# Optimization experiments

Measured on AMD Instinct MI355X. Metric: run time of the kernel, lower is better.

Reference implementation:

```python
import jax, jax.numpy as jnp
import numpy as np

T = 2048
HID = 5120
NH = 16
D_NOPE = 128
D_ROPE = 64
D_V = 128
Q_LORA = 1536
KV_LORA = 512
THETA = 10000.0
EPS = 1e-6
QK_HD = D_NOPE + D_ROPE
SCALE = QK_HD ** -0.5


def setup_inputs() -> dict:
    key = jax.random.key(0)
    ks = jax.random.split(key, 8)
    s = 0.02  # weight init scale for numerical stability
    return {
        "positions": jnp.arange(T, dtype=jnp.int32),
        "hidden_states": jax.random.normal(ks[0], (T, HID), jnp.float32),
        "w_qa": jax.random.normal(ks[1], (HID, Q_LORA), jnp.float32) * s,
        "qa_ln_w": jnp.ones((Q_LORA,), jnp.float32),
        "w_qb": jax.random.normal(ks[2], (Q_LORA, NH * QK_HD), jnp.float32) * s,
        "w_kva": jax.random.normal(ks[3], (HID, KV_LORA + D_ROPE), jnp.float32) * s,
        "kva_ln_w": jnp.ones((KV_LORA,), jnp.float32),
        "w_kvb": jax.random.normal(ks[4], (KV_LORA, NH * (D_NOPE + D_V)), jnp.float32) * s,
        "w_o": jax.random.normal(ks[5], (NH * D_V, HID), jnp.float32) * s,
    }


def rmsnorm(x, w):
    var = jnp.mean(x * x, axis=-1, keepdims=True)
    return x * jax.lax.rsqrt(var + EPS) * w


def apply_rope(positions, x):
    # GPT-J (interleaved) style rope on last dim of size D_ROPE; x: [T, H, D_ROPE]
    inv_freq = 1.0 / (THETA ** (jnp.arange(0, D_ROPE, 2, dtype=jnp.float32) / D_ROPE))
    ang = positions.astype(jnp.float32)[:, None] * inv_freq  # [T, D_ROPE/2]
    cos = jnp.cos(ang)[:, None, :]  # [T, 1, D/2]
    sin = jnp.sin(ang)[:, None, :]
    x1 = x[..., 0::2]
    x2 = x[..., 1::2]
    o1 = x1 * cos - x2 * sin
    o2 = x2 * cos + x1 * sin
    return jnp.stack([o1, o2], axis=-1).reshape(x.shape)


def reference(positions, hidden_states, w_qa, qa_ln_w, w_qb, w_kva, kva_ln_w, w_kvb, w_o):
    # --- low-rank Q path ---
    q_c = rmsnorm(hidden_states @ w_qa, qa_ln_w)             # [T, Q_LORA]
    q = (q_c @ w_qb).reshape(T, NH, QK_HD)                   # [T, H, 192]
    q_nope, q_pe = q[..., :D_NOPE], q[..., D_NOPE:]

    # --- compressed KV path ---
    kv = hidden_states @ w_kva                               # [T, KV_LORA + D_ROPE]
    kv_c = rmsnorm(kv[:, :KV_LORA], kva_ln_w)                # [T, 512]
    k_pe = kv[:, KV_LORA:][:, None, :]                       # [T, 1, 64]

    # partial rope
    q_pe = apply_rope(positions, q_pe)                       # [T, H, 64]
    k_pe = apply_rope(positions, k_pe)                       # [T, 1, 64]

    # decompress K_nope / V
    kv_up = (kv_c @ w_kvb).reshape(T, NH, D_NOPE + D_V)
    k_nope, v = kv_up[..., :D_NOPE], kv_up[..., D_NOPE:]     # [T, H, 128] each

    k_pe_b = jnp.broadcast_to(k_pe, (T, NH, D_ROPE))
    q_full = jnp.concatenate([q_nope, q_pe], axis=-1)        # [T, H, 192]
    k_full = jnp.concatenate([k_nope, k_pe_b], axis=-1)      # [T, H, 192]

    # causal attention
    scores = jnp.einsum("thd,shd->hts", q_full, k_full) * SCALE  # [H, T, T]
    causal = positions[:, None] >= positions[None, :]
    scores = jnp.where(causal[None], scores, jnp.finfo(scores.dtype).min)
    probs = jax.nn.softmax(scores, axis=-1)
    attn = jnp.einsum("hts,shd->thd", probs, v)              # [T, H, 128]

    out = attn.reshape(T, NH * D_V) @ w_o                    # [T, HID]
    return out
```

## Files before the change

kernel.cpp:

```cpp
#include <hip/hip_runtime.h>
#include <hip/hip_bf16.h>
#include <math.h>

#define T 2048
#define HID 5120
#define NH 16
#define D_NOPE 128
#define D_ROPE 64
#define D_V 128
#define Q_LORA 1536
#define KV_LORA 512
#define QK_HD 192
#define KVA_N 576
#define KVA_NP 640
#define N_QKVA (Q_LORA + KVA_NP)
#define N_QB (NH*QK_HD)
#define N_KVB (NH*(D_NOPE+D_V))
#define ATT_SCALE 0.07216878364870322f

typedef __bf16 bf16x8_t __attribute__((ext_vector_type(8)));
typedef float f32x4_t __attribute__((ext_vector_type(4)));
typedef unsigned short u16x4 __attribute__((ext_vector_type(4)));
typedef unsigned int u32x4 __attribute__((ext_vector_type(4)));

union BF8 { u16x4 h[2]; unsigned short u[8]; bf16x8_t v; u32x4 q; };

static __device__ __forceinline__ unsigned short f2bf(float f){
  union { float f; unsigned u; } x; x.f = f;
  unsigned r = x.u + 0x7FFFu + ((x.u >> 16) & 1u);
  return (unsigned short)(r >> 16);
}

static __device__ __forceinline__ void gload_lds16(const void* g, void* l){
  __builtin_amdgcn_global_load_lds(
      (const __attribute__((address_space(1))) void*)(unsigned long long)g,
      (__attribute__((address_space(3))) void*)(unsigned int)(unsigned long long)l,
      16, 0, 0);
}

__global__ __launch_bounds__(256) void k_cvt(const float* __restrict__ in,
                                             unsigned short* __restrict__ out, int n4){
  int i = blockIdx.x*256 + threadIdx.x;
  int stride = gridDim.x*256;
  for (; i < n4; i += stride){
    f32x4_t v = ((const f32x4_t*)in)[i];
    u16x4 o; o.x=f2bf(v.x); o.y=f2bf(v.y); o.z=f2bf(v.z); o.w=f2bf(v.w);
    ((u16x4*)out)[i] = o;
  }
}

__global__ __launch_bounds__(256) void k_cvtT(const float* __restrict__ W,
                                              unsigned short* __restrict__ Wt, int K, int N){
  __shared__ float tile[32][33];
  int n0 = blockIdx.x*32, k0 = blockIdx.y*32;
  int r = threadIdx.x >> 3, c4 = (threadIdx.x & 7) * 4;
  f32x4_t v = {0.f,0.f,0.f,0.f};
  if (n0 + c4 < N) v = *(const f32x4_t*)(W + (size_t)(k0 + r)*N + n0 + c4);
  tile[r][c4+0]=v.x; tile[r][c4+1]=v.y; tile[r][c4+2]=v.z; tile[r][c4+3]=v.w;
  __syncthreads();
  u16x4 o;
  o.x = f2bf(tile[c4+0][r]); o.y = f2bf(tile[c4+1][r]);
  o.z = f2bf(tile[c4+2][r]); o.w = f2bf(tile[c4+3][r]);
  *(u16x4*)(Wt + (size_t)(n0 + r)*K + k0 + c4) = o;
}

__global__ __launch_bounds__(256) void k_gemm(const unsigned short* __restrict__ A,
                                              const unsigned short* __restrict__ Bt,
                                              float* __restrict__ C,
                                              int M, int N, int K, int kChunk){
  __shared__ unsigned short sA[128*32];
  __shared__ unsigned short sB[128*32];
  int gx = gridDim.x;
  int nwg = gx*gridDim.y;
  int id = blockIdx.x + gx*blockIdx.y;
  int cpx = nwg >> 3;
  int swz = (id & 7)*cpx + (id >> 3);
  int bn = (swz % gx)*128, bm = (swz / gx)*128;
  int kBeg = blockIdx.z*kChunk;
  int kEnd = kBeg + kChunk; if (kEnd > K) kEnd = K;
  float* Cs = C + (size_t)blockIdx.z*M*N;
  int tid = threadIdx.x;
  int l = tid & 63, lr = l & 15, lg = l >> 4;
  int w = tid >> 6;
  int wm = (w >> 1)*64, wn = (w & 1)*64;
  f32x4_t acc[4][4];
  f32x4_t z4 = {0.f,0.f,0.f,0.f};
  #pragma unroll
  for (int i=0;i<4;i++)
    #pragma unroll
    for(int j=0;j<4;j++) acc[i][j] = z4;
  for (int k0 = kBeg; k0 < kEnd; k0 += 32){
    __syncthreads();
    #pragma unroll
    for (int it = 0; it < 2; ++it){
      int c = it*256 + tid;
      int row = c >> 2, kc = (c & 3) * 8;
      gload_lds16(A  + (size_t)(bm + row)*K + k0 + kc, &sA[c*8]);
      gload_lds16(Bt + (size_t)(bn + row)*K + k0 + kc, &sB[c*8]);
    }
    __syncthreads();
    BF8 af[4], bf[4];
    #pragma unroll
    for (int mf=0; mf<4; ++mf)
      af[mf].q = *(const u32x4*)&sA[(wm + mf*16 + lr)*32 + 8*lg];
    #pragma unroll
    for (int nf=0; nf<4; ++nf)
      bf[nf].q = *(const u32x4*)&sB[(wn + nf*16 + lr)*32 + 8*lg];
    #pragma unroll
    for (int mf=0; mf<4; ++mf)
      #pragma unroll
      for (int nf=0; nf<4; ++nf)
        acc[mf][nf] = __builtin_amdgcn_mfma_f32_16x16x32_bf16(af[mf].v, bf[nf].v, acc[mf][nf], 0,0,0);
  }
  #pragma unroll
  for (int mf=0; mf<4; ++mf){
    int row = bm + wm + mf*16 + 4*lg;
    #pragma unroll
    for (int nf=0; nf<4; ++nf){
      int col = bn + wn + nf*16 + lr;
      #pragma unroll
      for (int rg=0; rg<4; ++rg)
        Cs[(size_t)(row + rg)*N + col] = acc[mf][nf][rg];
    }
  }
}

__global__ __launch_bounds__(256) void k_red3(const float* __restrict__ P,
                                              float* __restrict__ out, int n4){
  const size_t sstr = (size_t)T*N_QKVA/4;
  int i = blockIdx.x*256 + threadIdx.x, stride = gridDim.x*256;
  const f32x4_t* p4 = (const f32x4_t*)P;
  f32x4_t* o4 = (f32x4_t*)out;
  for (; i < n4; i += stride)
    o4[i] = p4[i] + p4[i+sstr] + p4[i+2*sstr];
}

__global__ __launch_bounds__(256) void k_red_q(const float* __restrict__ P,
                                               const int* __restrict__ pos,
                                               unsigned short* __restrict__ q_full){
  int t = blockIdx.x, tid = threadIdx.x;
  const float* r0 = P + (size_t)t*N_QB;
  const float* r1 = r0 + (size_t)T*N_QB;
  float p = (float)pos[t];
  for (int idx = tid; idx < NH*160; idx += 256){
    int h = idx/160, j = idx - h*160;
    if (j < 128){
      float v = (r0[h*QK_HD + j] + r1[h*QK_HD + j]) * ATT_SCALE;
      q_full[((size_t)(h*T + t))*QK_HD + j] = f2bf(v);
    } else {
      int i = j - 128;
      int d0 = D_NOPE + 2*i;
      float x1 = r0[h*QK_HD + d0]   + r1[h*QK_HD + d0];
      float x2 = r0[h*QK_HD + d0+1] + r1[h*QK_HD + d0+1];
      float invf = 1.0f / powf(10000.0f, (float)(2*i)/64.0f);
      float sn, cs; sincosf(p*invf, &sn, &cs);
      unsigned short* qr = q_full + ((size_t)(h*T + t))*QK_HD + d0;
      qr[0] = f2bf((x1*cs - x2*sn)*ATT_SCALE);
      qr[1] = f2bf((x2*cs + x1*sn)*ATT_SCALE);
    }
  }
}

__global__ __launch_bounds__(256) void k_rms_q(const float* __restrict__ qkva,
                                               const float* __restrict__ w,
                                               unsigned short* __restrict__ qc){
  int t = blockIdx.x, tid = threadIdx.x;
  const float* row = qkva + (size_t)t*N_QKVA;
  float ss = 0.f;
  for (int i = tid; i < Q_LORA; i += 256){ float x = row[i]; ss += x*x; }
  #pragma unroll
  for (int off=1; off<64; off<<=1) ss += __shfl_xor(ss, off, 64);
  __shared__ float red[4];
  if ((tid & 63) == 0) red[tid>>6] = ss;
  __syncthreads();
  ss = red[0]+red[1]+red[2]+red[3];
  float sc = rsqrtf(ss/(float)Q_LORA + 1e-6f);
  unsigned short* orow = qc + (size_t)t*Q_LORA;
  for (int i = tid; i < Q_LORA; i += 256) orow[i] = f2bf(row[i]*sc*w[i]);
}

__global__ __launch_bounds__(256) void k_rms_kv(const float* __restrict__ qkva,
                                                const float* __restrict__ w,
                                                const int* __restrict__ pos,
                                                unsigned short* __restrict__ kvc,
                                                unsigned short* __restrict__ k_full){
  int t = blockIdx.x, tid = threadIdx.x;
  const float* row = qkva + (size_t)t*N_QKVA + Q_LORA;
  float ss = 0.f;
  for (int i = tid; i < KV_LORA; i += 256){ float x = row[i]; ss += x*x; }
  #pragma unroll
  for (int off=1; off<64; off<<=1) ss += __shfl_xor(ss, off, 64);
  __shared__ float red[4];
  if ((tid & 63) == 0) red[tid>>6] = ss;
  __syncthreads();
  ss = red[0]+red[1]+red[2]+red[3];
  float sc = rsqrtf(ss/(float)KV_LORA + 1e-6f);
  for (int i = tid; i < KV_LORA; i += 256)
    kvc[(size_t)t*KV_LORA + i] = f2bf(row[i]*sc*w[i]);
  if (tid < 32){
    int i = tid;
    float x1 = row[KV_LORA + 2*i], x2 = row[KV_LORA + 2*i + 1];
    float p = (float)pos[t];
    float invf = 1.0f / powf(10000.0f, (float)(2*i)/64.0f);
    float sn, cs; sincosf(p*invf, &sn, &cs);
    unsigned short b1 = f2bf(x1*cs - x2*sn), b2 = f2bf(x2*cs + x1*sn);
    for (int h=0; h<NH; ++h){
      unsigned short* kr = k_full + ((size_t)(h*T + t))*QK_HD + D_NOPE + 2*i;
      kr[0] = b1; kr[1] = b2;
    }
  }
}

__global__ __launch_bounds__(256) void k_scat_kv(const float* __restrict__ kvup,
                                                 unsigned short* __restrict__ k_full,
                                                 unsigned short* __restrict__ vt){
  int h = blockIdx.y, t0 = blockIdx.x*32;
  int tid = threadIdx.x;
  __shared__ float vtile[32][129];
  #pragma unroll
  for (int it=0; it<16; ++it){
    int idx = tid + it*256;
    int r = idx >> 7, d = idx & 127;
    float kn = kvup[(size_t)(t0 + r)*N_KVB + h*256 + d];
    k_full[((size_t)(h*T + t0 + r))*QK_HD + d] = f2bf(kn);
    vtile[r][d] = kvup[(size_t)(t0 + r)*N_KVB + h*256 + 128 + d];
  }
  __syncthreads();
  int d = tid >> 1, half = tid & 1;
  unsigned short* vrow = vt + ((size_t)(h*128 + d))*T + t0 + half*16;
  #pragma unroll
  for (int c=0; c<4; ++c){
    u16x4 o;
    o.x = f2bf(vtile[half*16 + c*4 + 0][d]);
    o.y = f2bf(vtile[half*16 + c*4 + 1][d]);
    o.z = f2bf(vtile[half*16 + c*4 + 2][d]);
    o.w = f2bf(vtile[half*16 + c*4 + 3][d]);
    *(u16x4*)(vrow + c*4) = o;
  }
}

__global__ __launch_bounds__(256,1) void k_attn(const unsigned short* __restrict__ q_full,
                                                const unsigned short* __restrict__ k_full,
                                                const unsigned short* __restrict__ vt,
                                                unsigned short* __restrict__ attn){
  __shared__ unsigned short K_lds[2][3*64*8*8];
  __shared__ unsigned short P_t[4][16][68];
  int bid = blockIdx.x;
  int h  = ((bid & 7) << 1) | ((bid >> 3) & 1);
  int qp = bid >> 4;
  int qtA = qp, qtB = 31 - qp;
  int ntiles = qtB + 1;
  int tid = threadIdx.x, w = tid >> 6, l = tid & 63, lr = l & 15, lg = l >> 4;
  int qrowA = qtA*64 + w*16 + lr;
  int qrowB = qtB*64 + w*16 + lr;
  BF8 qfA[6], qfB[6];
  {
    const unsigned short* qa = q_full + ((size_t)(h*T + qrowA))*QK_HD + 8*lg;
    const unsigned short* qb = q_full + ((size_t)(h*T + qrowB))*QK_HD + 8*lg;
    #pragma unroll
    for (int dk=0; dk<6; ++dk){
      qfA[dk].q = *(const u32x4*)(qa + dk*32);
      qfB[dk].q = *(const u32x4*)(qb + dk*32);
    }
  }
  float mA = -1e30f, lA = 0.f, mB = -1e30f, lB = 0.f;
  f32x4_t z4 = {0.f,0.f,0.f,0.f};
  f32x4_t oA[8], oB[8];
  #pragma unroll
  for (int i=0;i<8;i++){ oA[i] = z4; oB[i] = z4; }

  const unsigned short* kbase = k_full + (size_t)h*T*QK_HD;
  auto stageK = [&](int b, int t){
    #pragma unroll
    for (int is=0; is<6; ++is){
      int c = is*256 + tid;
      int chunk3 = c >> 9, row = (c >> 3) & 63, slot = c & 7;
      gload_lds16(kbase + (size_t)(t*64 + row)*QK_HD + chunk3*64 + ((slot ^ (row & 7))*8),
                  &K_lds[b][c*8]);
    }
  };
  stageK(0, 0);
  __syncthreads();
  int p = 0;
  int pslot0 = lg ^ (lr & 7), pslot1 = (4 + lg) ^ (lr & 7);
  for (int t = 0; t < ntiles; ++t){
    int s0 = t*64;
    BF8 va[8][2];
    #pragma unroll
    for (int df=0; df<8; ++df){
      const unsigned short* vp = vt + ((size_t)(h*D_V + df*16 + lr))*T + s0 + 8*lg;
      va[df][0].q = *(const u32x4*)(vp);
      va[df][1].q = *(const u32x4*)(vp + 32);
    }
    if (t+1 < ntiles) stageK(p^1, t+1);
    bool actA = (t <= qtA);
    f32x4_t sA[4], sB[4];
    #pragma unroll
    for (int i=0;i<4;i++){ sA[i] = z4; sB[i] = z4; }
    #pragma unroll
    for (int sfi=0; sfi<4; ++sfi){
      int rbase = (sfi*16 + lr)*8;
      #pragma unroll
      for (int dk=0; dk<6; ++dk){
        int ps = (dk & 1) ? pslot1 : pslot0;
        BF8 a; a.q = *(const u32x4*)&K_lds[p][(((dk>>1)*64*8) + rbase + ps)*8];
        sB[sfi] = __builtin_amdgcn_mfma_f32_16x16x32_bf16(a.v, qfB[dk].v, sB[sfi], 0,0,0);
        if (actA)
          sA[sfi] = __builtin_amdgcn_mfma_f32_16x16x32_bf16(a.v, qfA[dk].v, sA[sfi], 0,0,0);
      }
    }
    {
      bool diag = (t == ntiles-1);
      float tmax = -1e30f;
      #pragma unroll
      for (int sfi=0; sfi<4; ++sfi){
        #pragma unroll
        for (int rg=0; rg<4; ++rg){
          int s_g = s0 + sfi*16 + 4*lg + rg;
          float v = sB[sfi][rg];
          if (diag && s_g > qrowB) v = -1e30f;
          sB[sfi][rg] = v;
          tmax = fmaxf(tmax, v);
        }
      }
      tmax = fmaxf(tmax, __shfl_xor(tmax, 16, 64));
      tmax = fmaxf(tmax, __shfl_xor(tmax, 32, 64));
      float m_new = fmaxf(mB, tmax);
      float alpha = __expf(mB - m_new);
      float psum = 0.f;
      #pragma unroll
      for (int sfi=0; sfi<4; ++sfi){
        #pragma unroll
        for (int rg=0; rg<4; ++rg){
          float pv = __expf(sB[sfi][rg] - m_new);
          psum += pv;
          P_t[w][lr][sfi*16 + 4*lg + rg] = f2bf(pv);
        }
      }
      psum += __shfl_xor(psum, 16, 64);
      psum += __shfl_xor(psum, 32, 64);
      lB = lB*alpha + psum;
      mB = m_new;
      BF8 bp[2];
      #pragma unroll
      for (int ks=0; ks<2; ++ks){
        bp[ks].h[0] = *(const u16x4*)&P_t[w][lr][ks*32 + 8*lg];
        bp[ks].h[1] = *(const u16x4*)&P_t[w][lr][ks*32 + 8*lg + 4];
      }
      #pragma unroll
      for (int df=0; df<8; ++df){
        oB[df][0]*=alpha; oB[df][1]*=alpha; oB[df][2]*=alpha; oB[df][3]*=alpha;
        oB[df] = __builtin_amdgcn_mfma_f32_16x16x32_bf16(va[df][0].v, bp[0].v, oB[df], 0,0,0);
        oB[df] = __builtin_amdgcn_mfma_f32_16x16x32_bf16(va[df][1].v, bp[1].v, oB[df], 0,0,0);
      }
    }
    if (actA){
      bool diag = (t == qtA);
      float tmax = -1e30f;
      #pragma unroll
      for (int sfi=0; sfi<4; ++sfi){
        #pragma unroll
        for (int rg=0; rg<4; ++rg){
          int s_g = s0 + sfi*16 + 4*lg + rg;
          float v = sA[sfi][rg];
          if (diag && s_g > qrowA) v = -1e30f;
          sA[sfi][rg] = v;
          tmax = fmaxf(tmax, v);
        }
      }
      tmax = fmaxf(tmax, __shfl_xor(tmax, 16, 64));
      tmax = fmaxf(tmax, __shfl_xor(tmax, 32, 64));
      float m_new = fmaxf(mA, tmax);
      float alpha = __expf(mA - m_new);
      float psum = 0.f;
      #pragma unroll
      for (int sfi=0; sfi<4; ++sfi){
        #pragma unroll
        for (int rg=0; rg<4; ++rg){
          float pv = __expf(sA[sfi][rg] - m_new);
          psum += pv;
          P_t[w][lr][sfi*16 + 4*lg + rg] = f2bf(pv);
        }
      }
      psum += __shfl_xor(psum, 16, 64);
      psum += __shfl_xor(psum, 32, 64);
      lA = lA*alpha + psum;
      mA = m_new;
      BF8 bp[2];
      #pragma unroll
      for (int ks=0; ks<2; ++ks){
        bp[ks].h[0] = *(const u16x4*)&P_t[w][lr][ks*32 + 8*lg];
        bp[ks].h[1] = *(const u16x4*)&P_t[w][lr][ks*32 + 8*lg + 4];
      }
      #pragma unroll
      for (int df=0; df<8; ++df){
        oA[df][0]*=alpha; oA[df][1]*=alpha; oA[df][2]*=alpha; oA[df][3]*=alpha;
        oA[df] = __builtin_amdgcn_mfma_f32_16x16x32_bf16(va[df][0].v, bp[0].v, oA[df], 0,0,0);
        oA[df] = __builtin_amdgcn_mfma_f32_16x16x32_bf16(va[df][1].v, bp[1].v, oA[df], 0,0,0);
      }
    }
    __syncthreads();
    p ^= 1;
  }
  float invA = 1.0f / lA, invB = 1.0f / lB;
  #pragma unroll
  for (int df=0; df<8; ++df){
    u16x4 ov;
    ov.x = f2bf(oA[df][0]*invA); ov.y = f2bf(oA[df][1]*invA);
    ov.z = f2bf(oA[df][2]*invA); ov.w = f2bf(oA[df][3]*invA);
    *(u16x4*)(attn + (size_t)qrowA*(NH*D_V) + h*D_V + df*16 + 4*lg) = ov;
    ov.x = f2bf(oB[df][0]*invB); ov.y = f2bf(oB[df][1]*invB);
    ov.z = f2bf(oB[df][2]*invB); ov.w = f2bf(oB[df][3]*invB);
    *(u16x4*)(attn + (size_t)qrowB*(NH*D_V) + h*D_V + df*16 + 4*lg) = ov;
  }
}

extern "C" void kernel_launch(void* const* d_in, const int* in_sizes, int n_in,
                              void* d_out, int out_size, void* d_ws, size_t ws_size,
                              hipStream_t stream){
  const int*   positions = (const int*)d_in[0];
  const float* hidden = (const float*)d_in[1];
  const float* w_qa   = (const float*)d_in[2];
  const float* qa_ln  = (const float*)d_in[3];
  const float* w_qb   = (const float*)d_in[4];
  const float* w_kva  = (const float*)d_in[5];
  const float* kva_ln = (const float*)d_in[6];
  const float* w_kvb  = (const float*)d_in[7];
  const float* w_o    = (const float*)d_in[8];
  float* out = (float*)d_out;

  char* p = (char*)d_ws;
  auto alloc = [&](size_t bytes){ void* r = (void*)p; p += (bytes + 255) & ~(size_t)255; return r; };
  unsigned short* hb      = (unsigned short*)alloc((size_t)T*HID*2);
  unsigned short* wqkvaT  = (unsigned short*)alloc((size_t)N_QKVA*HID*2);
  unsigned short* wqbT    = (unsigned short*)alloc((size_t)N_QB*Q_LORA*2);
  unsigned short* wkvbT   = (unsigned short*)alloc((size_t)N_KVB*KV_LORA*2);
  unsigned short* woT     = (unsigned short*)alloc((size_t)HID*(NH*D_V)*2);
  float* qkva             = (float*)alloc((size_t)T*N_QKVA*4);
  unsigned short* q_c     = (unsigned short*)alloc((size_t)T*Q_LORA*2);
  unsigned short* kv_c    = (unsigned short*)alloc((size_t)T*KV_LORA*2);
  unsigned short* q_full  = (unsigned short*)alloc((size_t)NH*T*QK_HD*2);
  unsigned short* k_full  = (unsigned short*)alloc((size_t)NH*T*QK_HD*2);
  unsigned short* vt      = (unsigned short*)alloc((size_t)NH*D_V*T*2);
  unsigned short* attnb   = (unsigned short*)alloc((size_t)T*NH*D_V*2);
  float* Pbuf             = (float*)alloc((size_t)3*T*N_QKVA*4);
  float* kvupf            = Pbuf;

  k_cvt<<<2048, 256, 0, stream>>>(hidden, hb, T*HID/4);
  k_cvtT<<<dim3(Q_LORA/32, HID/32), 256, 0, stream>>>(w_qa, wqkvaT, HID, Q_LORA);
  k_cvtT<<<dim3(KVA_NP/32, HID/32), 256, 0, stream>>>(w_kva, wqkvaT + (size_t)Q_LORA*HID, HID, KVA_N);
  k_cvtT<<<dim3(N_QB/32, Q_LORA/32), 256, 0, stream>>>(w_qb, wqbT, Q_LORA, N_QB);
  k_cvtT<<<dim3(N_KVB/32, KV_LORA/32), 256, 0, stream>>>(w_kvb, wkvbT, KV_LORA, N_KVB);
  k_cvtT<<<dim3(HID/32, (NH*D_V)/32), 256, 0, stream>>>(w_o, woT, NH*D_V, HID);

  k_gemm<<<dim3(N_QKVA/128, T/128, 3), 256, 0, stream>>>(hb, wqkvaT, Pbuf, T, N_QKVA, HID, 1728);
  k_red3<<<1024, 256, 0, stream>>>(Pbuf, qkva, T*N_QKVA/4);
  k_rms_q<<<T, 256, 0, stream>>>(qkva, qa_ln, q_c);
  k_rms_kv<<<T, 256, 0, stream>>>(qkva, kva_ln, positions, kv_c, k_full);
  k_gemm<<<dim3(N_QB/128, T/128, 2), 256, 0, stream>>>(q_c, wqbT, Pbuf, T, N_QB, Q_LORA, 768);
  k_red_q<<<T, 256, 0, stream>>>(Pbuf, positions, q_full);
  k_gemm<<<dim3(N_KVB/128, T/128, 1), 256, 0, stream>>>(kv_c, wkvbT, kvupf, T, N_KVB, KV_LORA, KV_LORA);
  k_scat_kv<<<dim3(T/32, NH), 256, 0, stream>>>(kvupf, k_full, vt);
  k_attn<<<256, 256, 0, stream>>>(q_full, k_full, vt, attnb);
  k_gemm<<<dim3(HID/128, T/128, 1), 256, 0, stream>>>(attnb, woT, out, T, HID, NH*D_V, NH*D_V);
}
```

Baseline: 582.5 us.

## Split paired-tile attention blocks into single-tile blocks with lazy rescaling

```diff
diff --git a/kernel.cpp b/kernel.cpp
--- a/kernel.cpp
+++ b/kernel.cpp
@@ -239,35 +239,31 @@
   }
 }
 
-__global__ __launch_bounds__(256,1) void k_attn(const unsigned short* __restrict__ q_full,
+__global__ __launch_bounds__(256,2) void k_attn(const unsigned short* __restrict__ q_full,
                                                 const unsigned short* __restrict__ k_full,
                                                 const unsigned short* __restrict__ vt,
                                                 unsigned short* __restrict__ attn){
   __shared__ unsigned short K_lds[2][3*64*8*8];
   __shared__ unsigned short P_t[4][16][68];
   int bid = blockIdx.x;
-  int h  = ((bid & 7) << 1) | ((bid >> 3) & 1);
-  int qp = bid >> 4;
-  int qtA = qp, qtB = 31 - qp;
-  int ntiles = qtB + 1;
+  int half = bid >> 8, r = bid & 255;
+  int h  = ((r & 7) << 1) | ((r >> 3) & 1);
+  int qidx = r >> 4;
+  int qt = half ? (15 - qidx) : (31 - qidx);
+  int ntiles = qt + 1;
   int tid = threadIdx.x, w = tid >> 6, l = tid & 63, lr = l & 15, lg = l >> 4;
-  int qrowA = qtA*64 + w*16 + lr;
-  int qrowB = qtB*64 + w*16 + lr;
-  BF8 qfA[6], qfB[6];
+  int qrow = qt*64 + w*16 + lr;
+  BF8 qf[6];
   {
-    const unsigned short* qa = q_full + ((size_t)(h*T + qrowA))*QK_HD + 8*lg;
-    const unsigned short* qb = q_full + ((size_t)(h*T + qrowB))*QK_HD + 8*lg;
-    #pragma unroll
-    for (int dk=0; dk<6; ++dk){
-      qfA[dk].q = *(const u32x4*)(qa + dk*32);
-      qfB[dk].q = *(const u32x4*)(qb + dk*32);
-    }
-  }
-  float mA = -1e30f, lA = 0.f, mB = -1e30f, lB = 0.f;
+    const unsigned short* qp = q_full + ((size_t)(h*T + qrow))*QK_HD + 8*lg;
+    #pragma unroll
+    for (int dk=0; dk<6; ++dk) qf[dk].q = *(const u32x4*)(qp + dk*32);
+  }
+  float m_run = -1e30f, l_run = 0.f;
   f32x4_t z4 = {0.f,0.f,0.f,0.f};
-  f32x4_t oA[8], oB[8];
-  #pragma unroll
-  for (int i=0;i<8;i++){ oA[i] = z4; oB[i] = z4; }
+  f32x4_t o[8];
+  #pragma unroll
+  for (int i=0;i<8;i++) o[i] = z4;
 
   const unsigned short* kbase = k_full + (size_t)h*T*QK_HD;
   auto stageK = [&](int b, int t){
@@ -293,10 +289,10 @@
       va[df][1].q = *(const u32x4*)(vp + 32);
     }
     if (t+1 < ntiles) stageK(p^1, t+1);
-    bool actA = (t <= qtA);
-    f32x4_t sA[4], sB[4];
-    #pragma unroll
-    for (int i=0;i<4;i++){ sA[i] = z4; sB[i] = z4; }
+    f32x4_t sf[4];
+    #pragma unroll
+    for (int i=0;i<4;i++) sf[i] = z4;
+    __builtin_amdgcn_s_setprio(1);
     #pragma unroll
     for (int sfi=0; sfi<4; ++sfi){
       int rbase = (sfi*16 + lr)*8;
@@ -304,114 +300,72 @@
       for (int dk=0; dk<6; ++dk){
         int ps = (dk & 1) ? pslot1 : pslot0;
         BF8 a; a.q = *(const u32x4*)&K_lds[p][(((dk>>1)*64*8) + rbase + ps)*8];
-        sB[sfi] = __builtin_amdgcn_mfma_f32_16x16x32_bf16(a.v, qfB[dk].v, sB[sfi], 0,0,0);
-        if (actA)
-          sA[sfi] = __builtin_amdgcn_mfma_f32_16x16x32_bf16(a.v, qfA[dk].v, sA[sfi], 0,0,0);
+        sf[sfi] = __builtin_amdgcn_mfma_f32_16x16x32_bf16(a.v, qf[dk].v, sf[sfi], 0,0,0);
       }
     }
-    {
-      bool diag = (t == ntiles-1);
-      float tmax = -1e30f;
-      #pragma unroll
-      for (int sfi=0; sfi<4; ++sfi){
-        #pragma unroll
-        for (int rg=0; rg<4; ++rg){
-          int s_g = s0 + sfi*16 + 4*lg + rg;
-          float v = sB[sfi][rg];
-          if (diag && s_g > qrowB) v = -1e30f;
-          sB[sfi][rg] = v;
-          tmax = fmaxf(tmax, v);
-        }
+    __builtin_amdgcn_s_setprio(0);
+    bool diag = (t == ntiles-1);
+    float tmax = -1e30f;
+    #pragma unroll
+    for (int sfi=0; sfi<4; ++sfi){
+      #pragma unroll
+      for (int rg=0; rg<4; ++rg){
+        int s_g = s0 + sfi*16 + 4*lg + rg;
+        float v = sf[sfi][rg];
+        if (diag && s_g > qrow) v = -1e30f;
+        sf[sfi][rg] = v;
+        tmax = fmaxf(tmax, v);
       }
-      tmax = fmaxf(tmax, __shfl_xor(tmax, 16, 64));
-      tmax = fmaxf(tmax, __shfl_xor(tmax, 32, 64));
-      float m_new = fmaxf(mB, tmax);
-      float alpha = __expf(mB - m_new);
-      float psum = 0.f;
-      #pragma unroll
-      for (int sfi=0; sfi<4; ++sfi){
-        #pragma unroll
-        for (int rg=0; rg<4; ++rg){
-          float pv = __expf(sB[sfi][rg] - m_new);
-          psum += pv;
-          P_t[w][lr][sfi*16 + 4*lg + rg] = f2bf(pv);
-        }
+    }
+    tmax = fmaxf(tmax, __shfl_xor(tmax, 16, 64));
+    tmax = fmaxf(tmax, __shfl_xor(tmax, 32, 64));
+    bool norescale = __all(tmax - m_run <= 8.0f);
+    float alpha = 1.0f;
+    if (!norescale){
+      float m_new = fmaxf(m_run, tmax);
+      alpha = __expf(m_run - m_new);
+      m_run = m_new;
+    }
+    float psum = 0.f;
+    #pragma unroll
+    for (int sfi=0; sfi<4; ++sfi){
+      #pragma unroll
+      for (int rg=0; rg<4; ++rg){
+        float pv = __expf(sf[sfi][rg] - m_run);
+        psum += pv;
+        P_t[w][lr][sfi*16 + 4*lg + rg] = f2bf(pv);
       }
-      psum += __shfl_xor(psum, 16, 64);
-      psum += __shfl_xor(psum, 32, 64);
-      lB = lB*alpha + psum;
-      mB = m_new;
-      BF8 bp[2];
-      #pragma unroll
-      for (int ks=0; ks<2; ++ks){
-        bp[ks].h[0] = *(const u16x4*)&P_t[w][lr][ks*32 + 8*lg];
-        bp[ks].h[1] = *(const u16x4*)&P_t[w][lr][ks*32 + 8*lg + 4];
-      }
-      #pragma unroll
-      for (int df=0; df<8; ++df){
-        oB[df][0]*=alpha; oB[df][1]*=alpha; oB[df][2]*=alpha; oB[df][3]*=alpha;
-        oB[df] = __builtin_amdgcn_mfma_f32_16x16x32_bf16(va[df][0].v, bp[0].v, oB[df], 0,0,0);
-        oB[df] = __builtin_amdgcn_mfma_f32_16x16x32_bf16(va[df][1].v, bp[1].v, oB[df], 0,0,0);
-      }
-    }
-    if (actA){
-      bool diag = (t == qtA);
-      float tmax = -1e30f;
-      #pragma unroll
-      for (int sfi=0; sfi<4; ++sfi){
-        #pragma unroll
-        for (int rg=0; rg<4; ++rg){
-          int s_g = s0 + sfi*16 + 4*lg + rg;
-          float v = sA[sfi][rg];
-          if (diag && s_g > qrowA) v = -1e30f;
-          sA[sfi][rg] = v;
-          tmax = fmaxf(tmax, v);
-        }
-      }
-      tmax = fmaxf(tmax, __shfl_xor(tmax, 16, 64));
-      tmax = fmaxf(tmax, __shfl_xor(tmax, 32, 64));
-      float m_new = fmaxf(mA, tmax);
-      float alpha = __expf(mA - m_new);
-      float psum = 0.f;
-      #pragma unroll
-      for (int sfi=0; sfi<4; ++sfi){
-        #pragma unroll
-        for (int rg=0; rg<4; ++rg){
-          float pv = __expf(sA[sfi][rg] - m_new);
-          psum += pv;
-          P_t[w][lr][sfi*16 + 4*lg + rg] = f2bf(pv);
-        }
-      }
-      psum += __shfl_xor(psum, 16, 64);
-      psum += __shfl_xor(psum, 32, 64);
-      lA = lA*alpha + psum;
-      mA = m_new;
-      BF8 bp[2];
-      #pragma unroll
-      for (int ks=0; ks<2; ++ks){
-        bp[ks].h[0] = *(const u16x4*)&P_t[w][lr][ks*32 + 8*lg];
-        bp[ks].h[1] = *(const u16x4*)&P_t[w][lr][ks*32 + 8*lg + 4];
-      }
-      #pragma unroll
-      for (int df=0; df<8; ++df){
-        oA[df][0]*=alpha; oA[df][1]*=alpha; oA[df][2]*=alpha; oA[df][3]*=alpha;
-        oA[df] = __builtin_amdgcn_mfma_f32_16x16x32_bf16(va[df][0].v, bp[0].v, oA[df], 0,0,0);
-        oA[df] = __builtin_amdgcn_mfma_f32_16x16x32_bf16(va[df][1].v, bp[1].v, oA[df], 0,0,0);
-      }
-    }
+    }
+    psum += __shfl_xor(psum, 16, 64);
+    psum += __shfl_xor(psum, 32, 64);
+    l_run = l_run*alpha + psum;
+    if (!norescale){
+      #pragma unroll
+      for (int i=0;i<8;i++){ o[i][0]*=alpha; o[i][1]*=alpha; o[i][2]*=alpha; o[i][3]*=alpha; }
+    }
+    BF8 bp[2];
+    #pragma unroll
+    for (int ks=0; ks<2; ++ks){
+      bp[ks].h[0] = *(const u16x4*)&P_t[w][lr][ks*32 + 8*lg];
+      bp[ks].h[1] = *(const u16x4*)&P_t[w][lr][ks*32 + 8*lg + 4];
+    }
+    __builtin_amdgcn_s_setprio(1);
+    #pragma unroll
+    for (int df=0; df<8; ++df){
+      o[df] = __builtin_amdgcn_mfma_f32_16x16x32_bf16(va[df][0].v, bp[0].v, o[df], 0,0,0);
+      o[df] = __builtin_amdgcn_mfma_f32_16x16x32_bf16(va[df][1].v, bp[1].v, o[df], 0,0,0);
+    }
+    __builtin_amdgcn_s_setprio(0);
     __syncthreads();
     p ^= 1;
   }
-  float invA = 1.0f / lA, invB = 1.0f / lB;
+  float inv = 1.0f / l_run;
   #pragma unroll
   for (int df=0; df<8; ++df){
     u16x4 ov;
-    ov.x = f2bf(oA[df][0]*invA); ov.y = f2bf(oA[df][1]*invA);
-    ov.z = f2bf(oA[df][2]*invA); ov.w = f2bf(oA[df][3]*invA);
-    *(u16x4*)(attn + (size_t)qrowA*(NH*D_V) + h*D_V + df*16 + 4*lg) = ov;
-    ov.x = f2bf(oB[df][0]*invB); ov.y = f2bf(oB[df][1]*invB);
-    ov.z = f2bf(oB[df][2]*invB); ov.w = f2bf(oB[df][3]*invB);
-    *(u16x4*)(attn + (size_t)qrowB*(NH*D_V) + h*D_V + df*16 + 4*lg) = ov;
+    ov.x = f2bf(o[df][0]*inv); ov.y = f2bf(o[df][1]*inv);
+    ov.z = f2bf(o[df][2]*inv); ov.w = f2bf(o[df][3]*inv);
+    *(u16x4*)(attn + (size_t)qrow*(NH*D_V) + h*D_V + df*16 + 4*lg) = ov;
   }
 }
 
@@ -461,6 +415,6 @@
   k_red_q<<<T, 256, 0, stream>>>(Pbuf, positions, q_full);
   k_gemm<<<dim3(N_KVB/128, T/128, 1), 256, 0, stream>>>(kv_c, wkvbT, kvupf, T, N_KVB, KV_LORA, KV_LORA);
   k_scat_kv<<<dim3(T/32, NH), 256, 0, stream>>>(kvupf, k_full, vt);
-  k_attn<<<256, 256, 0, stream>>>(q_full, k_full, vt, attnb);
+  k_attn<<<512, 256, 0, stream>>>(q_full, k_full, vt, attnb);
   k_gemm<<<dim3(HID/128, T/128, 1), 256, 0, stream>>>(attnb, woT, out, T, HID, NH*D_V, NH*D_V);
 }
```

New measurement: 572.6 us. About the same (-1.7%).
